# Kernel optimization log

Measured on AMD Instinct MI355X. Metric: run time of the kernel, lower is better.

## Reference

```python
import jax, jax.numpy as jnp
import numpy as np

B, T, C, H = 4, 2048, 1024, 16
HS = C // H  # head size = 64


def setup_inputs() -> dict:
    key = jax.random.key(0)
    ks = jax.random.split(key, 9)
    s = 1.0 / np.sqrt(C)
    return {
        "x": jax.random.normal(ks[0], (B, T, C), dtype=jnp.float32),
        "Wq": jax.random.uniform(ks[1], (C, C), jnp.float32, -s, s),
        "bq": jax.random.uniform(ks[2], (C,), jnp.float32, -s, s),
        "Wk": jax.random.uniform(ks[3], (C, C), jnp.float32, -s, s),
        "bk": jax.random.uniform(ks[4], (C,), jnp.float32, -s, s),
        "Wv": jax.random.uniform(ks[5], (C, C), jnp.float32, -s, s),
        "bv": jax.random.uniform(ks[6], (C,), jnp.float32, -s, s),
        "Wp": jax.random.uniform(ks[7], (C, C), jnp.float32, -s, s),
        "bp": jax.random.uniform(ks[8], (C,), jnp.float32, -s, s),
    }


def reference(x, Wq, bq, Wk, bk, Wv, bv, Wp, bp):
    Bx, Tx, Cx = x.shape
    # QKV projections -> [B, H, T, HS]
    def heads(w, b):
        return (x @ w.T + b).reshape(Bx, Tx, H, HS).transpose(0, 2, 1, 3)
    q = heads(Wq, bq)
    k = heads(Wk, bk)
    v = heads(Wv, bv)
    scale = 1.0 / np.sqrt(HS).astype(np.float32)
    att = jnp.einsum("bhqd,bhkd->bhqk", q, k) * scale  # [B,H,T,T]
    causal = jnp.tril(jnp.ones((Tx, Tx), dtype=bool))
    att = jnp.where(causal[None, None], att, -jnp.inf)
    att = jax.nn.softmax(att, axis=-1)
    y = jnp.einsum("bhqk,bhkd->bhqd", att, v)  # [B,H,T,HS]
    y = y.transpose(0, 2, 1, 3).reshape(Bx, Tx, Cx)
    return y @ Wp.T + bp
```

## Files before the change

### kernel.cpp

```cpp
#include <hip/hip_runtime.h>
#include <hip/hip_bf16.h>

typedef __hip_bfloat16 bf16;
typedef __attribute__((ext_vector_type(8))) short bf16x8;
typedef __attribute__((ext_vector_type(4))) float f32x4;

#define B_  4
#define T_  2048
#define C_  1024
#define H_  16
#define HS_ 64
#define M_  (B_ * T_)

__device__ __forceinline__ short f2bf(float x) {
    bf16 h = __float2bfloat16(x);
    return *reinterpret_cast<short*>(&h);
}
__device__ __forceinline__ unsigned pk2(float lo, float hi) {
    return ((unsigned)(unsigned short)f2bf(hi) << 16) | (unsigned short)f2bf(lo);
}

__device__ __forceinline__ unsigned pk2a(float lo, float hi) {
    unsigned r;
    asm("v_cvt_pk_bf16_f32 %0, %1, %2" : "=v"(r) : "v"(lo), "v"(hi));
    return r;
}

__device__ __forceinline__ float fast_exp2(float x) {
#if __has_builtin(__builtin_amdgcn_exp2f)
    return __builtin_amdgcn_exp2f(x);
#else
    return exp2f(x);
#endif
}

__device__ __forceinline__ void async16(void* lds, const void* g) {
    __builtin_amdgcn_global_load_lds(
        (const __attribute__((address_space(1))) unsigned int*)g,
        (__attribute__((address_space(3))) unsigned int*)lds, 16, 0, 0);
}

#define CV_S0 1048576u
#define CV_S1 (CV_S0 + 393216u)
#define CV_S2 (CV_S1 + 131072u)
#define CV_S3 (CV_S2 + 384u)

__global__ __launch_bounds__(256) void convert_kernel(
    const float* __restrict__ x,
    const float* __restrict__ Wq, const float* __restrict__ Wk,
    const float* __restrict__ Wv, const float* __restrict__ Wp,
    const float* __restrict__ bq, const float* __restrict__ bk,
    const float* __restrict__ bv,
    bf16* __restrict__ xb, bf16* __restrict__ wqkv, bf16* __restrict__ wpb,
    float* __restrict__ bqkv)
{
    const unsigned idx = blockIdx.x * 256u + threadIdx.x;
    if (idx >= CV_S3) return;

    const float* src;
    bf16* dst;
    size_t soff, doff;
    if (idx < CV_S0) {
        soff = (size_t)idx * 8; doff = soff; src = x; dst = xb;
    } else if (idx < CV_S1) {
        const size_t e0 = (size_t)(idx - CV_S0) * 8;
        const int row = (int)(e0 >> 10);
        const int col = (int)(e0 & 1023);
        src = (row < 1024) ? Wq : (row < 2048) ? Wk : Wv;
        soff = ((size_t)(row & 1023) << 10) + col;
        doff = e0; dst = wqkv;
    } else if (idx < CV_S2) {
        soff = (size_t)(idx - CV_S1) * 8; doff = soff; src = Wp; dst = wpb;
    } else {
        const int e0 = (int)(idx - CV_S2) * 8;
        #pragma unroll
        for (int e = 0; e < 8; e++) {
            const int n = e0 + e;
            bqkv[n] = (n < 1024) ? bq[n] : (n < 2048) ? bk[n - 1024] : bv[n - 2048];
        }
        return;
    }

    const float4 a = *(const float4*)(src + soff);
    const float4 b = *(const float4*)(src + soff + 4);
    uint4 o;
    o.x = pk2(a.x, a.y);
    o.y = pk2(a.z, a.w);
    o.z = pk2(b.x, b.y);
    o.w = pk2(b.z, b.w);
    *(uint4*)(dst + doff) = o;
}

template <int QKV>
__global__ __launch_bounds__(256) void gemm_mfma(const bf16* __restrict__ A,
                                                 const bf16* __restrict__ W,
                                                 const float* __restrict__ bias,
                                                 bf16* __restrict__ qo,
                                                 bf16* __restrict__ ko,
                                                 bf16* __restrict__ vo,
                                                 float* __restrict__ out)
{
    __shared__ __align__(16) short As[128 * 64];
    __shared__ __align__(16) short Bs[128 * 64];

    const int tid  = threadIdx.x;
    const int lane = tid & 63;
    const int w    = tid >> 6;
    const int l15  = lane & 15;
    const int quad = lane >> 4;
    const int xs = (blockIdx.x & 7) * ((int)gridDim.x >> 3) + (blockIdx.x >> 3);
    const int m0 = xs * 128;
    const int n0 = blockIdx.y * 128;
    const int wm = (w & 1) * 64;
    const int wn = (w >> 1) * 64;

    f32x4 acc[4][4];
    #pragma unroll
    for (int i = 0; i < 4; i++)
        #pragma unroll
        for (int j = 0; j < 4; j++)
            acc[i][j] = (f32x4){0.f, 0.f, 0.f, 0.f};

    const int srow   = lane >> 3;
    const int schunk = (lane & 7) ^ srow;

    for (int k0 = 0; k0 < C_; k0 += 64) {
        #pragma unroll
        for (int i = 0; i < 4; i++) {
            const int r0 = w * 32 + i * 8;
            async16(&As[r0 * 64],
                    A + (size_t)(m0 + r0 + srow) * C_ + k0 + schunk * 8);
            async16(&Bs[r0 * 64],
                    W + (size_t)(n0 + r0 + srow) * C_ + k0 + schunk * 8);
        }
        __syncthreads();

        #pragma unroll
        for (int kc = 0; kc < 2; kc++) {
            const int swz = ((kc * 4 + quad) ^ (l15 & 7)) * 8;
            bf16x8 af[4], bfr[4];
            #pragma unroll
            for (int mi = 0; mi < 4; mi++)
                af[mi] = *(const bf16x8*)&As[(wm + mi * 16 + l15) * 64 + swz];
            #pragma unroll
            for (int ni = 0; ni < 4; ni++)
                bfr[ni] = *(const bf16x8*)&Bs[(wn + ni * 16 + l15) * 64 + swz];
            #pragma unroll
            for (int mi = 0; mi < 4; mi++)
                #pragma unroll
                for (int ni = 0; ni < 4; ni++)
                    acc[mi][ni] = __builtin_amdgcn_mfma_f32_16x16x32_bf16(
                        af[mi], bfr[ni], acc[mi][ni], 0, 0, 0);
        }
        __syncthreads();
    }

    #pragma unroll
    for (int mi = 0; mi < 4; mi++) {
        #pragma unroll
        for (int r = 0; r < 4; r++) {
            const int m  = m0 + wm + mi * 16 + quad * 4 + r;
            const int bb = m >> 11;
            const int tt = m & (T_ - 1);
            #pragma unroll
            for (int ni = 0; ni < 4; ni++) {
                const int n = n0 + wn + ni * 16 + l15;
                const float val = acc[mi][ni][r] + bias[n];
                if (QKV) {
                    const int sel = n >> 10;
                    const int nn  = n & 1023;
                    const int hh  = nn >> 6;
                    const int dd  = nn & 63;
                    bf16* dst = (sel == 0) ? qo : (sel == 1) ? ko : vo;
                    dst[(((size_t)(bb * H_ + hh) * T_ + tt) << 6) + dd] =
                        __float2bfloat16(val);
                } else {
                    out[((size_t)m << 10) + n] = val;
                }
            }
        }
    }
}

__global__ __launch_bounds__(256) void transpose_v(const bf16* __restrict__ V,
                                                   bf16* __restrict__ Vt)
{
    __shared__ __align__(16) short tile[64 * 72];

    const int t0 = blockIdx.x * 64;
    const int h = blockIdx.y, b = blockIdx.z;
    const size_t base = ((size_t)(b * H_ + h) * T_) << 6;

    const int tr = threadIdx.x & 63;
    const int dc = (threadIdx.x >> 6) * 16;
    const bf16x8 a = *(const bf16x8*)(V + base + (size_t)(t0 + tr) * 64 + dc);
    const bf16x8 c = *(const bf16x8*)(V + base + (size_t)(t0 + tr) * 64 + dc + 8);
    #pragma unroll
    for (int e = 0; e < 8; e++) {
        tile[(dc + e) * 72 + tr]     = a[e];
        tile[(dc + 8 + e) * 72 + tr] = c[e];
    }
    __syncthreads();

    const int d  = threadIdx.x >> 2;
    const int tc = (threadIdx.x & 3) * 16;
    const bf16x8 o0 = *(const bf16x8*)&tile[d * 72 + tc];
    const bf16x8 o1 = *(const bf16x8*)&tile[d * 72 + tc + 8];
    *(bf16x8*)(Vt + base + (size_t)d * T_ + t0 + tc)     = o0;
    *(bf16x8*)(Vt + base + (size_t)d * T_ + t0 + tc + 8) = o1;
}

#define LOG2E_X_SCALE 0.18033688011112042f
#define LOG2E_X_BIAS  -34.62468098133513f

__global__ __launch_bounds__(256) void attn_bal(const bf16* __restrict__ Q,
                                                const bf16* __restrict__ K,
                                                const bf16* __restrict__ Vt,
                                                bf16* __restrict__ Y)
{
    __shared__ __align__(16) short Pl[4][64 * 72];

    const int tid  = threadIdx.x;
    const int lane = tid & 63;
    const int w    = tid >> 6;
    const int l15  = lane & 15;
    const int quad = lane >> 4;

    const unsigned bid  = blockIdx.x;
    const unsigned orig = ((bid & 7u) << 6) | (bid >> 3);
    const int bx = orig & 7;
    const int h  = (orig >> 3) & 15;
    const int b  = (int)(orig >> 7);
    const size_t base = ((size_t)(b * H_ + h) * T_) << 6;

    const int g  = bx * 4 + w;
    const int qf = g * 32;
    const int qm = T_ - 32 - qf;
    const int r0[4] = {qf, qf + 16, qm, qm + 16};
    const int ntf = ((qf + 31) >> 6) + 1;
    const int ntm = ((qm + 31) >> 6) + 1;

    bf16x8 qfr[4][2];
    #pragma unroll
    for (int qn = 0; qn < 4; qn++)
        #pragma unroll
        for (int ch = 0; ch < 2; ch++)
            qfr[qn][ch] = *(const bf16x8*)(Q + base +
                (size_t)(r0[qn] + l15) * 64 + ch * 32 + quad * 8);

    f32x4 acc[4][4];
    #pragma unroll
    for (int dt = 0; dt < 4; dt++)
        #pragma unroll
        for (int qn = 0; qn < 4; qn++)
            acc[dt][qn] = (f32x4){0.f, 0.f, 0.f, 0.f};
    float lsum[4] = {0.f, 0.f, 0.f, 0.f};

    short* myP = &Pl[w][0];

    for (int t = 0; t < ntm; t++) {
        const int j0 = t << 6;
        const bool fact = (t < ntf);

        #pragma unroll
        for (int kt = 0; kt < 4; kt++) {
            const size_t krow = base + (size_t)(j0 + kt * 16 + l15) * 64 + quad * 8;
            const bf16x8 kf0 = *(const bf16x8*)(K + krow);
            const bf16x8 kf1 = *(const bf16x8*)(K + krow + 32);
            #pragma unroll
            for (int qn = 0; qn < 4; qn++) {
                if (qn < 2 && !fact) continue;
                f32x4 s = (f32x4){0.f, 0.f, 0.f, 0.f};
                s = __builtin_amdgcn_mfma_f32_16x16x32_bf16(kf0, qfr[qn][0], s, 0, 0, 0);
                s = __builtin_amdgcn_mfma_f32_16x16x32_bf16(kf1, qfr[qn][1], s, 0, 0, 0);
                const int r0q = r0[qn];
                const bool msk = (j0 + 63 > r0q);
                float p[4];
                #pragma unroll
                for (int r = 0; r < 4; r++) {
                    float e = fast_exp2(fmaf(s[r], LOG2E_X_SCALE, LOG2E_X_BIAS));
                    if (msk) {
                        const int key = j0 + kt * 16 + quad * 4 + r;
                        e = (key <= r0q + l15) ? e : 0.f;
                    }
                    p[r] = e;
                    lsum[qn] += e;
                }
                uint2 pkd;
                pkd.x = pk2a(p[0], p[1]);
                pkd.y = pk2a(p[2], p[3]);
                *(uint2*)&myP[(qn * 16 + l15) * 72 + kt * 16 + quad * 4] = pkd;
            }
        }

        #pragma unroll
        for (int ch = 0; ch < 2; ch++) {
            bf16x8 pf[4];
            #pragma unroll
            for (int qn = 0; qn < 4; qn++)
                if (qn >= 2 || fact)
                    pf[qn] = *(const bf16x8*)&myP[(qn * 16 + l15) * 72 + ch * 32 + quad * 8];
            #pragma unroll
            for (int dt = 0; dt < 4; dt++) {
                const bf16x8 vf = *(const bf16x8*)(Vt + base +
                    (size_t)(dt * 16 + l15) * T_ + j0 + ch * 32 + quad * 8);
                #pragma unroll
                for (int qn = 0; qn < 4; qn++)
                    if (qn >= 2 || fact)
                        acc[dt][qn] = __builtin_amdgcn_mfma_f32_16x16x32_bf16(
                            vf, pf[qn], acc[dt][qn], 0, 0, 0);
            }
        }
    }

    #pragma unroll
    for (int qn = 0; qn < 4; qn++) {
        lsum[qn] += __shfl_xor(lsum[qn], 16, 64);
        lsum[qn] += __shfl_xor(lsum[qn], 32, 64);
    }

    #pragma unroll
    for (int qn = 0; qn < 4; qn++) {
        const float inv = 1.f / lsum[qn];
        const int tt = r0[qn] + l15;
        bf16* yrow = Y + (((size_t)(b * T_ + tt)) << 10) + (h << 6);
        #pragma unroll
        for (int dt = 0; dt < 4; dt++) {
            uint2 o;
            o.x = pk2a(acc[dt][qn][0] * inv, acc[dt][qn][1] * inv);
            o.y = pk2a(acc[dt][qn][2] * inv, acc[dt][qn][3] * inv);
            *(uint2*)(yrow + dt * 16 + quad * 4) = o;
        }
    }
}

__global__ void zero_out_kernel(float* out, size_t n) {
    const size_t i = (size_t)blockIdx.x * 256 + threadIdx.x;
    if (i < n) out[i] = 0.f;
}

extern "C" void kernel_launch(void* const* d_in, const int* in_sizes, int n_in,
                              void* d_out, int out_size, void* d_ws, size_t ws_size,
                              hipStream_t stream)
{
    const float* x  = (const float*)d_in[0];
    const float* Wq = (const float*)d_in[1];
    const float* bq = (const float*)d_in[2];
    const float* Wk = (const float*)d_in[3];
    const float* bk = (const float*)d_in[4];
    const float* Wv = (const float*)d_in[5];
    const float* bv = (const float*)d_in[6];
    const float* Wp = (const float*)d_in[7];
    const float* bp = (const float*)d_in[8];

    const size_t nElem = (size_t)M_ * C_;

    size_t off = 0;
    auto alloc = [&](size_t bytes) {
        void* p = (char*)d_ws + off;
        off += (bytes + 255) & ~(size_t)255;
        return p;
    };
    bf16*  xb   = (bf16*)alloc(nElem * 2);
    bf16*  q    = (bf16*)alloc(nElem * 2);
    bf16*  k    = (bf16*)alloc(nElem * 2);
    bf16*  v    = (bf16*)alloc(nElem * 2);
    bf16*  wqkv = (bf16*)alloc((size_t)3 * C_ * C_ * 2);
    bf16*  wpb  = (bf16*)alloc((size_t)C_ * C_ * 2);
    float* bqkv = (float*)alloc(3 * C_ * 4);

    if (off > ws_size) {
        const size_t n = (size_t)out_size;
        zero_out_kernel<<<(int)((n + 255) / 256), 256, 0, stream>>>((float*)d_out, n);
        return;
    }

    convert_kernel<<<(CV_S3 + 255) / 256, 256, 0, stream>>>(
        x, Wq, Wk, Wv, Wp, bq, bk, bv, xb, wqkv, wpb, bqkv);

    gemm_mfma<1><<<dim3(M_ / 128, 3 * C_ / 128), 256, 0, stream>>>(
        xb, wqkv, bqkv, q, k, v, nullptr);

    bf16* vt = xb;
    transpose_v<<<dim3(T_ / 64, H_, B_), 256, 0, stream>>>(v, vt);

    bf16* y = v;
    attn_bal<<<dim3(512), 256, 0, stream>>>(q, k, vt, y);

    gemm_mfma<0><<<dim3(M_ / 128, C_ / 128), 256, 0, stream>>>(
        y, wpb, bp, nullptr, nullptr, nullptr, (float*)d_out);
}
```

Measured before the change: 325.3 us.

## Stage K and V tiles in shared memory with double-buffered async loads

The attention kernel now cooperatively loads each 64-key K tile and V^T tile into XOR-swizzled shared memory with async copies, double-buffering so the next tile prefetches while the current one is computed. Each wave previously read K and V directly from global memory on its own. The four waves now share a single load, and the swizzle is meant to avoid LDS bank conflicts. In exchange the block iterates to the longest wave's tile count with a __syncthreads per tile, which adds barrier and idle cost for waves that have less work, and it uses 32 KB more LDS, which may lower occupancy.

```diff
diff --git a/kernel.cpp b/kernel.cpp
--- a/kernel.cpp
+++ b/kernel.cpp
@@ -219,6 +219,8 @@
                                                 bf16* __restrict__ Y)
 {
     __shared__ __align__(16) short Pl[4][64 * 72];
+    __shared__ __align__(16) short Ks[2][64 * 64];
+    __shared__ __align__(16) short Vs[2][64 * 64];
 
     const int tid  = threadIdx.x;
     const int lane = tid & 63;
@@ -239,6 +241,7 @@
     const int r0[4] = {qf, qf + 16, qm, qm + 16};
     const int ntf = ((qf + 31) >> 6) + 1;
     const int ntm = ((qm + 31) >> 6) + 1;
+    const int ntmax = ((2047 - 128 * bx) >> 6) + 1;
 
     bf16x8 qfr[4][2];
     #pragma unroll
@@ -258,59 +261,92 @@
 
     short* myP = &Pl[w][0];
 
-    for (int t = 0; t < ntm; t++) {
+    const int srow   = lane >> 3;
+    const int schunk = (lane & 7) ^ srow;
+    const int myrow  = l15 & 7;
+
+    #pragma unroll
+    for (int i = 0; i < 2; i++) {
+        const int r0s = w * 16 + i * 8;
+        async16(&Ks[0][r0s * 64],
+                K + base + (size_t)(r0s + srow) * 64 + schunk * 8);
+        async16(&Vs[0][r0s * 64],
+                Vt + base + (size_t)(r0s + srow) * T_ + schunk * 8);
+    }
+    __syncthreads();
+
+    int cur = 0;
+    for (int t = 0; t < ntmax; t++) {
         const int j0 = t << 6;
-        const bool fact = (t < ntf);
-
-        #pragma unroll
-        for (int kt = 0; kt < 4; kt++) {
-            const size_t krow = base + (size_t)(j0 + kt * 16 + l15) * 64 + quad * 8;
-            const bf16x8 kf0 = *(const bf16x8*)(K + krow);
-            const bf16x8 kf1 = *(const bf16x8*)(K + krow + 32);
-            #pragma unroll
-            for (int qn = 0; qn < 4; qn++) {
-                if (qn < 2 && !fact) continue;
-                f32x4 s = (f32x4){0.f, 0.f, 0.f, 0.f};
-                s = __builtin_amdgcn_mfma_f32_16x16x32_bf16(kf0, qfr[qn][0], s, 0, 0, 0);
-                s = __builtin_amdgcn_mfma_f32_16x16x32_bf16(kf1, qfr[qn][1], s, 0, 0, 0);
-                const int r0q = r0[qn];
-                const bool msk = (j0 + 63 > r0q);
-                float p[4];
+
+        if (t + 1 < ntmax) {
+            const int j0n = j0 + 64;
+            #pragma unroll
+            for (int i = 0; i < 2; i++) {
+                const int r0s = w * 16 + i * 8;
+                async16(&Ks[cur ^ 1][r0s * 64],
+                        K + base + (size_t)(j0n + r0s + srow) * 64 + schunk * 8);
+                async16(&Vs[cur ^ 1][r0s * 64],
+                        Vt + base + (size_t)(r0s + srow) * T_ + j0n + schunk * 8);
+            }
+        }
+
+        if (t < ntm) {
+            const bool fact = (t < ntf);
+
+            #pragma unroll
+            for (int kt = 0; kt < 4; kt++) {
+                const int krow = (kt * 16 + l15) * 64;
+                const bf16x8 kf0 = *(const bf16x8*)&Ks[cur][krow + ((quad ^ myrow) * 8)];
+                const bf16x8 kf1 = *(const bf16x8*)&Ks[cur][krow + (((4 + quad) ^ myrow) * 8)];
                 #pragma unroll
-                for (int r = 0; r < 4; r++) {
-                    float e = fast_exp2(fmaf(s[r], LOG2E_X_SCALE, LOG2E_X_BIAS));
-                    if (msk) {
-                        const int key = j0 + kt * 16 + quad * 4 + r;
-                        e = (key <= r0q + l15) ? e : 0.f;
+                for (int qn = 0; qn < 4; qn++) {
+                    if (qn < 2 && !fact) continue;
+                    f32x4 s = (f32x4){0.f, 0.f, 0.f, 0.f};
+                    s = __builtin_amdgcn_mfma_f32_16x16x32_bf16(kf0, qfr[qn][0], s, 0, 0, 0);
+                    s = __builtin_amdgcn_mfma_f32_16x16x32_bf16(kf1, qfr[qn][1], s, 0, 0, 0);
+                    const int r0q = r0[qn];
+                    const bool msk = (j0 + 63 > r0q);
+                    float p[4];
+                    #pragma unroll
+                    for (int r = 0; r < 4; r++) {
+                        float e = fast_exp2(fmaf(s[r], LOG2E_X_SCALE, LOG2E_X_BIAS));
+                        if (msk) {
+                            const int key = j0 + kt * 16 + quad * 4 + r;
+                            e = (key <= r0q + l15) ? e : 0.f;
+                        }
+                        p[r] = e;
+                        lsum[qn] += e;
                     }
-                    p[r] = e;
-                    lsum[qn] += e;
+                    uint2 pkd;
+                    pkd.x = pk2a(p[0], p[1]);
+                    pkd.y = pk2a(p[2], p[3]);
+                    *(uint2*)&myP[(qn * 16 + l15) * 72 + kt * 16 + quad * 4] = pkd;
                 }
-                uint2 pkd;
-                pkd.x = pk2a(p[0], p[1]);
-                pkd.y = pk2a(p[2], p[3]);
-                *(uint2*)&myP[(qn * 16 + l15) * 72 + kt * 16 + quad * 4] = pkd;
             }
-        }
-
-        #pragma unroll
-        for (int ch = 0; ch < 2; ch++) {
-            bf16x8 pf[4];
-            #pragma unroll
-            for (int qn = 0; qn < 4; qn++)
-                if (qn >= 2 || fact)
-                    pf[qn] = *(const bf16x8*)&myP[(qn * 16 + l15) * 72 + ch * 32 + quad * 8];
-            #pragma unroll
-            for (int dt = 0; dt < 4; dt++) {
-                const bf16x8 vf = *(const bf16x8*)(Vt + base +
-                    (size_t)(dt * 16 + l15) * T_ + j0 + ch * 32 + quad * 8);
+
+            #pragma unroll
+            for (int ch = 0; ch < 2; ch++) {
+                bf16x8 pf[4];
                 #pragma unroll
                 for (int qn = 0; qn < 4; qn++)
                     if (qn >= 2 || fact)
-                        acc[dt][qn] = __builtin_amdgcn_mfma_f32_16x16x32_bf16(
-                            vf, pf[qn], acc[dt][qn], 0, 0, 0);
+                        pf[qn] = *(const bf16x8*)&myP[(qn * 16 + l15) * 72 + ch * 32 + quad * 8];
+                #pragma unroll
+                for (int dt = 0; dt < 4; dt++) {
+                    const bf16x8 vf = *(const bf16x8*)
+                        &Vs[cur][(dt * 16 + l15) * 64 + (((ch * 4 + quad) ^ myrow) * 8)];
+                    #pragma unroll
+                    for (int qn = 0; qn < 4; qn++)
+                        if (qn >= 2 || fact)
+                            acc[dt][qn] = __builtin_amdgcn_mfma_f32_16x16x32_bf16(
+                                vf, pf[qn], acc[dt][qn], 0, 0, 0);
+                }
             }
         }
+
+        __syncthreads();
+        cur ^= 1;
     }
 
     #pragma unroll
```

Measured after the change: 276.4 us. -15.0%, faster.
